# Optimization experiments

Measured on AMD Instinct MI355X. Metric: run time of the kernel, lower is better.

Reference implementation:

```python
import jax, jax.numpy as jnp
import numpy as np

N_CELLS = 100000
IN_CH = 64
N_EDGES = 1280000


def setup_inputs() -> dict:
    key = jax.random.key(0)
    k1, k2, k3, k4, k5 = jax.random.split(key, 5)
    x_source = jax.random.normal(k1, (N_CELLS, IN_CH), dtype=jnp.float32)
    att_weight = jax.random.normal(k2, (2 * IN_CH,), dtype=jnp.float32)
    nbhd_values = jax.random.uniform(k3, (N_EDGES,), dtype=jnp.float32)
    target_index_i = jnp.sort(jax.random.randint(k4, (N_EDGES,), 0, N_CELLS))
    source_index_j = jax.random.randint(k5, (N_EDGES,), 0, N_CELLS)
    return {
        "x_source": x_source,
        "att_weight": att_weight,
        "nbhd_values": nbhd_values,
        "target_index_i": target_index_i,
        "source_index_j": source_index_j,
    }


def reference(x_source, att_weight, nbhd_values, target_index_i, source_index_j):
    # gather per-message endpoint features: [E, C] each
    x_src_msg = x_source[source_index_j]
    x_tgt_msg = x_source[target_index_i]  # x_target is None -> use x_source
    # attention: elu(cat([src, tgt]) @ w) -> [E]
    att = jax.nn.elu(
        jnp.concatenate([x_src_msg, x_tgt_msg], axis=1) @ att_weight
    )
    # modulate sparse neighborhood values by attention, scale messages
    vals = nbhd_values * att  # [E]
    x_message = vals[:, None] * x_src_msg  # [E, C]
    # scatter-sum into target cells: [N, C]
    return jax.ops.segment_sum(x_message, target_index_i, num_segments=N_CELLS)
```

## Files before the change

### kernel.cpp

```cpp
#include <hip/hip_runtime.h>

#define N_CELLS 100000
#define IN_CH 64
#define N_EDGES 1280000

__device__ __forceinline__ unsigned short f32_to_bf16(float f) {
    unsigned u = __float_as_uint(f);
    u += 0x7FFFu + ((u >> 16) & 1u);
    return (unsigned short)(u >> 16);
}
__device__ __forceinline__ float bf16_to_f32(unsigned short h) {
    return __uint_as_float((unsigned)h << 16);
}

__global__ void __launch_bounds__(256) score_kernel(
    const float* __restrict__ x, const float* __restrict__ w,
    float* __restrict__ s_src, float* __restrict__ s_tgt,
    unsigned short* __restrict__ xb, int n_cells) {
    int gid  = blockIdx.x * blockDim.x + threadIdx.x;
    int wave = gid >> 6;
    int lane = threadIdx.x & 63;
    int grp  = lane >> 4;
    int sub  = lane & 15;
    int cell = wave * 4 + grp;

    float4 xv = make_float4(0.f, 0.f, 0.f, 0.f);
    if (cell < n_cells)
        xv = *(const float4*)&x[(((unsigned)cell << 6) | ((unsigned)sub << 2))];
    if (xb && cell < n_cells) {
        ushort4 hb;
        hb.x = f32_to_bf16(xv.x); hb.y = f32_to_bf16(xv.y);
        hb.z = f32_to_bf16(xv.z); hb.w = f32_to_bf16(xv.w);
        *(ushort4*)&xb[(((unsigned)cell << 6) | ((unsigned)sub << 2))] = hb;
    }
    const float4* w4 = (const float4*)w;
    float4 wa = w4[sub];
    float4 wb = w4[16 + sub];
    float a = xv.x * wa.x + xv.y * wa.y + xv.z * wa.z + xv.w * wa.w;
    float b = xv.x * wb.x + xv.y * wb.y + xv.z * wb.z + xv.w * wb.w;
#pragma unroll
    for (int off = 8; off; off >>= 1) {
        a += __shfl_xor(a, off, 64);
        b += __shfl_xor(b, off, 64);
    }
    if (sub == 0 && cell < n_cells) {
        s_src[cell] = a;
        s_tgt[cell] = b;
    }
}

__global__ void __launch_bounds__(256) rowstart_kernel(
    const int* __restrict__ tgt, int* __restrict__ row_start,
    int n_edges, int n_cells) {
    int e = blockIdx.x * blockDim.x + threadIdx.x;
    if (e >= n_edges) return;
    int lane = threadIdx.x & 63;
    int t = tgt[e];
    int prev = __shfl_up(t, 1, 64);
    if (lane == 0) prev = (e == 0) ? -1 : tgt[e - 1];
    for (int c = prev + 1; c <= t; ++c) row_start[c] = e;
    if (e == n_edges - 1) {
        for (int c = t + 1; c <= n_cells; ++c) row_start[c] = n_edges;
    }
}

__global__ void __launch_bounds__(256) agg_kernel_bf16(
    const unsigned short* __restrict__ xb, const int* __restrict__ src,
    const float* __restrict__ nbhd,
    const float* __restrict__ s_src, const float* __restrict__ s_tgt,
    const int* __restrict__ row_start,
    float* __restrict__ out, int n_cells) {
    int gid  = blockIdx.x * blockDim.x + threadIdx.x;
    int lane = threadIdx.x & 63;
    int grp  = lane >> 4;
    int sub  = lane & 15;
    int cell = (gid >> 6) * 4 + grp;
    unsigned suboff = (unsigned)sub << 2;
    int gbase = grp << 4;

    int lo = 0, hi = 0;
    float sti = 0.f;
    if (cell < n_cells) {
        lo  = row_start[cell];
        hi  = row_start[cell + 1];
        sti = s_tgt[cell];
    }

    float4 acc = make_float4(0.f, 0.f, 0.f, 0.f);
    for (int base = lo; base < hi; base += 16) {
        int cnt = hi - base;
        if (cnt > 16) cnt = 16;
        int   j = 0;
        float v = 0.f;
        if (sub < cnt) {
            j = src[base + sub];
            float a = s_src[j] + sti;
            v = nbhd[base + sub] * (a > 0.f ? a : expm1f(a));
        }
        int t = 0;
        for (; t + 4 <= cnt; t += 4) {
            int   j0 = __shfl(j, gbase + t,     64);
            int   j1 = __shfl(j, gbase + t + 1, 64);
            int   j2 = __shfl(j, gbase + t + 2, 64);
            int   j3 = __shfl(j, gbase + t + 3, 64);
            float v0 = __shfl(v, gbase + t,     64);
            float v1 = __shfl(v, gbase + t + 1, 64);
            float v2 = __shfl(v, gbase + t + 2, 64);
            float v3 = __shfl(v, gbase + t + 3, 64);
            ushort4 h0 = *(const ushort4*)&xb[(((unsigned)j0 << 6) | suboff)];
            ushort4 h1 = *(const ushort4*)&xb[(((unsigned)j1 << 6) | suboff)];
            ushort4 h2 = *(const ushort4*)&xb[(((unsigned)j2 << 6) | suboff)];
            ushort4 h3 = *(const ushort4*)&xb[(((unsigned)j3 << 6) | suboff)];
            acc.x = fmaf(v0, bf16_to_f32(h0.x), acc.x);
            acc.y = fmaf(v0, bf16_to_f32(h0.y), acc.y);
            acc.z = fmaf(v0, bf16_to_f32(h0.z), acc.z);
            acc.w = fmaf(v0, bf16_to_f32(h0.w), acc.w);
            acc.x = fmaf(v1, bf16_to_f32(h1.x), acc.x);
            acc.y = fmaf(v1, bf16_to_f32(h1.y), acc.y);
            acc.z = fmaf(v1, bf16_to_f32(h1.z), acc.z);
            acc.w = fmaf(v1, bf16_to_f32(h1.w), acc.w);
            acc.x = fmaf(v2, bf16_to_f32(h2.x), acc.x);
            acc.y = fmaf(v2, bf16_to_f32(h2.y), acc.y);
            acc.z = fmaf(v2, bf16_to_f32(h2.z), acc.z);
            acc.w = fmaf(v2, bf16_to_f32(h2.w), acc.w);
            acc.x = fmaf(v3, bf16_to_f32(h3.x), acc.x);
            acc.y = fmaf(v3, bf16_to_f32(h3.y), acc.y);
            acc.z = fmaf(v3, bf16_to_f32(h3.z), acc.z);
            acc.w = fmaf(v3, bf16_to_f32(h3.w), acc.w);
        }
        for (; t < cnt; ++t) {
            int   jt = __shfl(j, gbase + t, 64);
            float vt = __shfl(v, gbase + t, 64);
            ushort4 ht = *(const ushort4*)&xb[(((unsigned)jt << 6) | suboff)];
            acc.x = fmaf(vt, bf16_to_f32(ht.x), acc.x);
            acc.y = fmaf(vt, bf16_to_f32(ht.y), acc.y);
            acc.z = fmaf(vt, bf16_to_f32(ht.z), acc.z);
            acc.w = fmaf(vt, bf16_to_f32(ht.w), acc.w);
        }
    }
    if (cell < n_cells)
        *(float4*)&out[(((unsigned)cell << 6) | suboff)] = acc;
}

__global__ void __launch_bounds__(256) agg_kernel_f32(
    const float* __restrict__ x, const int* __restrict__ src,
    const float* __restrict__ nbhd,
    const float* __restrict__ s_src, const float* __restrict__ s_tgt,
    const int* __restrict__ row_start,
    float* __restrict__ out, int n_cells) {
    int gid  = blockIdx.x * blockDim.x + threadIdx.x;
    int lane = threadIdx.x & 63;
    int grp  = lane >> 4;
    int sub  = lane & 15;
    int cell = (gid >> 6) * 4 + grp;
    unsigned suboff = (unsigned)sub << 2;
    int gbase = grp << 4;

    int lo = 0, hi = 0;
    float sti = 0.f;
    if (cell < n_cells) {
        lo  = row_start[cell];
        hi  = row_start[cell + 1];
        sti = s_tgt[cell];
    }
    float4 acc = make_float4(0.f, 0.f, 0.f, 0.f);
    for (int base = lo; base < hi; base += 16) {
        int cnt = hi - base;
        if (cnt > 16) cnt = 16;
        int   j = 0;
        float v = 0.f;
        if (sub < cnt) {
            j = src[base + sub];
            float a = s_src[j] + sti;
            v = nbhd[base + sub] * (a > 0.f ? a : expm1f(a));
        }
        for (int t = 0; t < cnt; ++t) {
            int   jt = __shfl(j, gbase + t, 64);
            float vt = __shfl(v, gbase + t, 64);
            float4 xt = *(const float4*)&x[(((unsigned)jt << 6) | suboff)];
            acc.x = fmaf(vt, xt.x, acc.x); acc.y = fmaf(vt, xt.y, acc.y);
            acc.z = fmaf(vt, xt.z, acc.z); acc.w = fmaf(vt, xt.w, acc.w);
        }
    }
    if (cell < n_cells)
        *(float4*)&out[(((unsigned)cell << 6) | suboff)] = acc;
}

extern "C" void kernel_launch(void* const* d_in, const int* in_sizes, int n_in,
                              void* d_out, int out_size, void* d_ws, size_t ws_size,
                              hipStream_t stream) {
    const float* x    = (const float*)d_in[0];
    const float* w    = (const float*)d_in[1];
    const float* nbhd = (const float*)d_in[2];
    const int*   tgt  = (const int*)d_in[3];
    const int*   src  = (const int*)d_in[4];
    float*       out  = (float*)d_out;

    float* s_src     = (float*)d_ws;
    float* s_tgt     = s_src + N_CELLS;
    int*   row_start = (int*)(s_tgt + N_CELLS);
    unsigned short* xb = (unsigned short*)(row_start + N_CELLS + 1);
    size_t need_bf16 = (size_t)(2 * N_CELLS + N_CELLS + 1) * 4 + (size_t)N_CELLS * IN_CH * 2;
    bool use_bf16 = ws_size >= need_bf16;

    {
        int threads = 256;
        int blocks  = (N_CELLS * 16 + threads - 1) / threads;
        score_kernel<<<blocks, threads, 0, stream>>>(x, w, s_src, s_tgt,
                                                     use_bf16 ? xb : (unsigned short*)nullptr,
                                                     N_CELLS);
    }
    {
        int threads = 256;
        int blocks  = (N_EDGES + threads - 1) / threads;
        rowstart_kernel<<<blocks, threads, 0, stream>>>(tgt, row_start, N_EDGES, N_CELLS);
    }
    {
        int threads = 256;
        int blocks  = (N_CELLS * 16 + threads - 1) / threads;
        if (use_bf16)
            agg_kernel_bf16<<<blocks, threads, 0, stream>>>(xb, src, nbhd, s_src, s_tgt,
                                                            row_start, out, N_CELLS);
        else
            agg_kernel_f32<<<blocks, threads, 0, stream>>>(x, src, nbhd, s_src, s_tgt,
                                                           row_start, out, N_CELLS);
    }
}
```

Before: 63.07 us.

## Merge score and rowstart kernels; bitonic-sort neighbor indices per chunk

Fuses the score/bf16-conversion kernel and the row-start kernel into one launch, with block ranges picking the role. This saves one launch and lets the two independent passes overlap. In the aggregation kernel, each 16-edge chunk's source indices and weights are bitonic-sorted across the 16 lanes before the gathers, so gathers run in ascending address order for better cache/TLB locality. The sort adds about 20 shuffle pairs per chunk, which may outweigh any locality gain for random indices.

Measured after the change: 62.08 us. No clear change (-1.6%).

```diff
diff --git a/kernel.cpp b/kernel.cpp
--- a/kernel.cpp
+++ b/kernel.cpp
@@ -13,54 +13,57 @@
     return __uint_as_float((unsigned)h << 16);
 }
 
-__global__ void __launch_bounds__(256) score_kernel(
+#define SCORE_BLOCKS ((N_CELLS * 16 + 255) / 256)
+#define ROWSTART_BLOCKS ((N_EDGES + 255) / 256)
+
+__global__ void __launch_bounds__(256) prep_kernel(
     const float* __restrict__ x, const float* __restrict__ w,
+    const int* __restrict__ tgt,
     float* __restrict__ s_src, float* __restrict__ s_tgt,
-    unsigned short* __restrict__ xb, int n_cells) {
-    int gid  = blockIdx.x * blockDim.x + threadIdx.x;
-    int wave = gid >> 6;
-    int lane = threadIdx.x & 63;
-    int grp  = lane >> 4;
-    int sub  = lane & 15;
-    int cell = wave * 4 + grp;
-
-    float4 xv = make_float4(0.f, 0.f, 0.f, 0.f);
-    if (cell < n_cells)
-        xv = *(const float4*)&x[(((unsigned)cell << 6) | ((unsigned)sub << 2))];
-    if (xb && cell < n_cells) {
-        ushort4 hb;
-        hb.x = f32_to_bf16(xv.x); hb.y = f32_to_bf16(xv.y);
-        hb.z = f32_to_bf16(xv.z); hb.w = f32_to_bf16(xv.w);
-        *(ushort4*)&xb[(((unsigned)cell << 6) | ((unsigned)sub << 2))] = hb;
-    }
-    const float4* w4 = (const float4*)w;
-    float4 wa = w4[sub];
-    float4 wb = w4[16 + sub];
-    float a = xv.x * wa.x + xv.y * wa.y + xv.z * wa.z + xv.w * wa.w;
-    float b = xv.x * wb.x + xv.y * wb.y + xv.z * wb.z + xv.w * wb.w;
+    unsigned short* __restrict__ xb, int* __restrict__ row_start,
+    int n_cells, int n_edges) {
+    if (blockIdx.x < SCORE_BLOCKS) {
+        int gid  = blockIdx.x * 256 + threadIdx.x;
+        int wave = gid >> 6;
+        int lane = threadIdx.x & 63;
+        int grp  = lane >> 4;
+        int sub  = lane & 15;
+        int cell = wave * 4 + grp;
+
+        float4 xv = make_float4(0.f, 0.f, 0.f, 0.f);
+        if (cell < n_cells)
+            xv = *(const float4*)&x[(((unsigned)cell << 6) | ((unsigned)sub << 2))];
+        if (xb && cell < n_cells) {
+            ushort4 hb;
+            hb.x = f32_to_bf16(xv.x); hb.y = f32_to_bf16(xv.y);
+            hb.z = f32_to_bf16(xv.z); hb.w = f32_to_bf16(xv.w);
+            *(ushort4*)&xb[(((unsigned)cell << 6) | ((unsigned)sub << 2))] = hb;
+        }
+        const float4* w4 = (const float4*)w;
+        float4 wa = w4[sub];
+        float4 wb = w4[16 + sub];
+        float a = xv.x * wa.x + xv.y * wa.y + xv.z * wa.z + xv.w * wa.w;
+        float b = xv.x * wb.x + xv.y * wb.y + xv.z * wb.z + xv.w * wb.w;
 #pragma unroll
-    for (int off = 8; off; off >>= 1) {
-        a += __shfl_xor(a, off, 64);
-        b += __shfl_xor(b, off, 64);
-    }
-    if (sub == 0 && cell < n_cells) {
-        s_src[cell] = a;
-        s_tgt[cell] = b;
-    }
-}
-
-__global__ void __launch_bounds__(256) rowstart_kernel(
-    const int* __restrict__ tgt, int* __restrict__ row_start,
-    int n_edges, int n_cells) {
-    int e = blockIdx.x * blockDim.x + threadIdx.x;
-    if (e >= n_edges) return;
-    int lane = threadIdx.x & 63;
-    int t = tgt[e];
-    int prev = __shfl_up(t, 1, 64);
-    if (lane == 0) prev = (e == 0) ? -1 : tgt[e - 1];
-    for (int c = prev + 1; c <= t; ++c) row_start[c] = e;
-    if (e == n_edges - 1) {
-        for (int c = t + 1; c <= n_cells; ++c) row_start[c] = n_edges;
+        for (int off = 8; off; off >>= 1) {
+            a += __shfl_xor(a, off, 64);
+            b += __shfl_xor(b, off, 64);
+        }
+        if (sub == 0 && cell < n_cells) {
+            s_src[cell] = a;
+            s_tgt[cell] = b;
+        }
+    } else {
+        int e = (blockIdx.x - SCORE_BLOCKS) * 256 + threadIdx.x;
+        if (e >= n_edges) return;
+        int lane = threadIdx.x & 63;
+        int t = tgt[e];
+        int prev = __shfl_up(t, 1, 64);
+        if (lane == 0) prev = (e == 0) ? -1 : tgt[e - 1];
+        for (int c = prev + 1; c <= t; ++c) row_start[c] = e;
+        if (e == n_edges - 1) {
+            for (int c = t + 1; c <= n_cells; ++c) row_start[c] = n_edges;
+        }
     }
 }
 
@@ -90,13 +93,26 @@
     for (int base = lo; base < hi; base += 16) {
         int cnt = hi - base;
         if (cnt > 16) cnt = 16;
-        int   j = 0;
-        float v = 0.f;
+        int   key = 0x7FFFFFFF;
+        float v   = 0.f;
         if (sub < cnt) {
-            j = src[base + sub];
+            int j = src[base + sub];
             float a = s_src[j] + sti;
             v = nbhd[base + sub] * (a > 0.f ? a : expm1f(a));
-        }
+            key = j;
+        }
+#pragma unroll
+        for (int size = 2; size <= 16; size <<= 1) {
+#pragma unroll
+            for (int strd = size >> 1; strd > 0; strd >>= 1) {
+                int   pk = __shfl_xor(key, strd, 64);
+                float pv = __shfl_xor(v,   strd, 64);
+                bool takeMin = ((sub & size) == 0) == ((sub & strd) == 0);
+                bool sw = takeMin ? (pk < key) : (pk > key);
+                if (sw) { key = pk; v = pv; }
+            }
+        }
+        int j = key;
         int t = 0;
         for (; t + 4 <= cnt; t += 4) {
             int   j0 = __shfl(j, gbase + t,     64);
@@ -204,16 +220,10 @@
     bool use_bf16 = ws_size >= need_bf16;
 
     {
-        int threads = 256;
-        int blocks  = (N_CELLS * 16 + threads - 1) / threads;
-        score_kernel<<<blocks, threads, 0, stream>>>(x, w, s_src, s_tgt,
-                                                     use_bf16 ? xb : (unsigned short*)nullptr,
-                                                     N_CELLS);
-    }
-    {
-        int threads = 256;
-        int blocks  = (N_EDGES + threads - 1) / threads;
-        rowstart_kernel<<<blocks, threads, 0, stream>>>(tgt, row_start, N_EDGES, N_CELLS);
+        int blocks = SCORE_BLOCKS + ROWSTART_BLOCKS;
+        prep_kernel<<<blocks, 256, 0, stream>>>(x, w, tgt, s_src, s_tgt,
+                                                use_bf16 ? xb : (unsigned short*)nullptr,
+                                                row_start, N_CELLS, N_EDGES);
     }
     {
         int threads = 256;
```
